# Kernel optimization log

Hardware: AMD Instinct MI355X
Metric: run time of the kernel (lower is better)

The kernel has to match this reference:

```python
import jax, jax.numpy as jnp
import numpy as np


def setup_inputs() -> dict:
    key = jax.random.key(0)
    k1, k2, k3, k4 = jax.random.split(key, 4)
    B, C, H, Wd = 32, 512, 32, 32
    sparse_dim, dict_size, feature_dim = 1024, 1024, 512
    x = jax.random.normal(k1, (B, C, H, Wd), dtype=jnp.float32)
    dictionary = jax.random.normal(k2, (dict_size, feature_dim), dtype=jnp.float32)
    # scale W, S like the LISTA init (|| . || ~ O(1)) so iterates stay bounded
    W = jax.random.normal(k3, (sparse_dim, feature_dim), dtype=jnp.float32) * 0.02
    S = jax.random.normal(k4, (sparse_dim, sparse_dim), dtype=jnp.float32) * 0.02
    thresh = jnp.float32(0.1)
    return {"x": x, "dictionary": dictionary, "W": W, "S": S, "thresh": thresh, "num_steps": 5}


def _soft_threshold(z, thresh):
    return jnp.sign(z) * jnp.maximum(jnp.abs(z) - thresh, 0.0)


def reference(x, dictionary, W, S, thresh, num_steps):
    B, C, H, Wd = x.shape
    sparse_dim = S.shape[0]
    # [B,C,H,W] -> [B*H*W, C]
    x_flat = jnp.transpose(x, (0, 2, 3, 1)).reshape(-1, C)
    dict_norm = dictionary / jnp.linalg.norm(dictionary, axis=1, keepdims=True)
    # W @ x^T is loop-invariant; compute once. [K, N]
    Wx = W @ x_flat.T
    z = jnp.zeros((sparse_dim, x_flat.shape[0]), dtype=x.dtype)
    for _ in range(num_steps):
        z = z + Wx
        z = z - S @ z
        z = _soft_threshold(z, thresh)
    # [K,N] -> [B,K,H,W]
    z = jnp.transpose(z.T.reshape(B, H, Wd, sparse_dim), (0, 3, 1, 2))
    return (z, dict_norm)
```

## Files before the change

### kernel.cpp

```cpp
#include <hip/hip_runtime.h>
#include <hip/hip_bf16.h>

typedef __bf16 bf16_t;
typedef __bf16 bf16x4 __attribute__((ext_vector_type(4)));
typedef __bf16 bf16x8 __attribute__((ext_vector_type(8)));
typedef float f32x4 __attribute__((ext_vector_type(4)));

#define GLOAD_LDS16(g, l)                                                      \
  __builtin_amdgcn_global_load_lds(                                            \
      (const __attribute__((address_space(1))) void*)(g),                      \
      (__attribute__((address_space(3))) void*)(l), 16, 0, 0)

#define MFMA(a, b, c) __builtin_amdgcn_mfma_f32_16x16x32_bf16((a), (b), (c), 0, 0, 0)

__global__ __launch_bounds__(512, 2) void gemm_kernel(
    const bf16_t* __restrict__ A, const bf16_t* __restrict__ Bt,
    int Kd, int mode,
    const bf16_t* __restrict__ WxIn, bf16_t* __restrict__ UnextOrWx,
    float* __restrict__ Out, const float* __restrict__ thresh_p)
{
  __shared__ __align__(16) char smem[147456];
  bf16_t* lds = (bf16_t*)smem;

  const int tid = threadIdx.x;
  const int wid = tid >> 6, lane = tid & 63;
  const int wr = wid >> 1, wc = wid & 1;
  const int lr = lane & 15, kg = lane >> 4;

  const int per = gridDim.x >> 3;
  const int logical = (blockIdx.x & 7) * per + (blockIdx.x >> 3);
  const int tileN = (logical & 7) << 7;
  const int tileM = (logical >> 3) << 8;
  const int NT = Kd >> 6;

  size_t offA[4]; int dstA[4];
  #pragma unroll
  for (int j = 0; j < 4; ++j) {
    const int f = j * 512 + tid;
    const int row = f >> 3, u = f & 7;
    const int ug = u ^ (row & 7);
    offA[j] = (size_t)(tileM + row) * Kd + ug * 8;
    dstA[j] = f * 8;
  }
  size_t offB[2]; int dstB[2];
  #pragma unroll
  for (int j = 0; j < 2; ++j) {
    const int f = j * 512 + tid;
    const int col = f >> 3, u = f & 7;
    const int ug = u ^ (col & 7);
    offB[j] = (size_t)(tileN + col) * Kd + ug * 8;
    dstB[j] = 16384 + f * 8;
  }

  auto readA = [&](int mi, int ks, int bs) -> bf16x8 {
    const int R = wr * 64 + mi * 16 + lr;
    const int ul = (ks * 4 + kg) ^ (R & 7);
    return *(const bf16x8*)(lds + bs + R * 64 + ul * 8);
  };
  auto readB = [&](int ni, int ks, int bs) -> bf16x8 {
    const int C = wc * 64 + ni * 16 + lr;
    const int ul = (ks * 4 + kg) ^ (C & 7);
    return *(const bf16x8*)(lds + bs + 16384 + C * 64 + ul * 8);
  };

  f32x4 acc[4][4] = {};
  bf16x8 af[4], bfr[4];

  #pragma unroll
  for (int j = 0; j < 4; ++j) GLOAD_LDS16(A + offA[j], lds + dstA[j]);
  #pragma unroll
  for (int j = 0; j < 2; ++j) GLOAD_LDS16(Bt + offB[j], lds + dstB[j]);
  if (NT > 1) {
    #pragma unroll
    for (int j = 0; j < 4; ++j) GLOAD_LDS16(A + offA[j] + 64, lds + 24576 + dstA[j]);
    #pragma unroll
    for (int j = 0; j < 2; ++j) GLOAD_LDS16(Bt + offB[j] + 64, lds + 24576 + dstB[j]);
  }
  asm volatile("s_waitcnt vmcnt(6)" ::: "memory");
  __builtin_amdgcn_s_barrier();

  int buf = 0, sb3 = 2;
  for (int t = 0; t < NT; ++t) {
    const int bs = buf * 24576;
    const int sbs = sb3 * 24576;
    const int ts = (t + 2 < NT) ? t + 2 : t + 2 - NT;
    const size_t ko = (size_t)ts << 6;

    #pragma unroll
    for (int mi = 0; mi < 4; ++mi) af[mi] = readA(mi, 0, bs);
    #pragma unroll
    for (int ni = 0; ni < 4; ++ni) bfr[ni] = readB(ni, 0, bs);
    GLOAD_LDS16(A + offA[0] + ko, lds + sbs + dstA[0]);
    GLOAD_LDS16(A + offA[1] + ko, lds + sbs + dstA[1]);
    GLOAD_LDS16(A + offA[2] + ko, lds + sbs + dstA[2]);
    __builtin_amdgcn_s_barrier();
    asm volatile("s_waitcnt lgkmcnt(0)" ::: "memory");
    __builtin_amdgcn_sched_barrier(0);
    __builtin_amdgcn_s_setprio(1);
    #pragma unroll
    for (int mi = 0; mi < 4; ++mi)
      #pragma unroll
      for (int ni = 0; ni < 4; ++ni)
        acc[mi][ni] = MFMA(af[mi], bfr[ni], acc[mi][ni]);
    __builtin_amdgcn_s_setprio(0);

    #pragma unroll
    for (int mi = 0; mi < 4; ++mi) af[mi] = readA(mi, 1, bs);
    #pragma unroll
    for (int ni = 0; ni < 4; ++ni) bfr[ni] = readB(ni, 1, bs);
    GLOAD_LDS16(A + offA[3] + ko, lds + sbs + dstA[3]);
    GLOAD_LDS16(Bt + offB[0] + ko, lds + sbs + dstB[0]);
    GLOAD_LDS16(Bt + offB[1] + ko, lds + sbs + dstB[1]);
    __builtin_amdgcn_s_barrier();
    asm volatile("s_waitcnt lgkmcnt(0)" ::: "memory");
    __builtin_amdgcn_sched_barrier(0);
    __builtin_amdgcn_s_setprio(1);
    #pragma unroll
    for (int mi = 0; mi < 4; ++mi)
      #pragma unroll
      for (int ni = 0; ni < 4; ++ni)
        acc[mi][ni] = MFMA(af[mi], bfr[ni], acc[mi][ni]);
    __builtin_amdgcn_s_setprio(0);
    asm volatile("s_waitcnt vmcnt(6)" ::: "memory");
    __builtin_amdgcn_s_barrier();

    buf = (buf == 2) ? 0 : buf + 1;
    sb3 = (sb3 == 2) ? 0 : sb3 + 1;
  }

  const float th = *thresh_p;

  if (mode <= 1) {
    asm volatile("s_waitcnt vmcnt(0)" ::: "memory");
    __syncthreads();
    float* Tl = (float*)smem;
    #pragma unroll
    for (int c = 0; c < 8; ++c) {
      if (c) __syncthreads();
      if (wr == (c >> 1)) {
        #pragma unroll
        for (int mj = 0; mj < 2; ++mj) {
          const int mi = (c & 1) * 2 + mj;
          const int rl = mj * 16 + kg * 4;
          #pragma unroll
          for (int ni = 0; ni < 4; ++ni) {
            const int cl = wc * 64 + ni * 16 + lr;
            #pragma unroll
            for (int r = 0; r < 4; ++r)
              Tl[(rl + r) * 132 + cl] = acc[mi][ni][r];
          }
        }
      }
      __syncthreads();
      #pragma unroll
      for (int j = 0; j < 2; ++j) {
        const int f  = j * 512 + tid;
        const int rl = f >> 5;
        const int c4 = (f & 31) * 4;
        const f32x4 v = *(const f32x4*)&Tl[rl * 132 + c4];
        const int grow = tileM + c * 32 + rl;
        const size_t gidx = (size_t)grow * 1024 + tileN + c4;
        bf16x4 ov;
        if (mode == 1) {
          const bf16x4 wx = *(const bf16x4*)&WxIn[gidx];
          #pragma unroll
          for (int e = 0; e < 4; ++e) {
            const float a  = fabsf(v[e]) - th;
            const float zn = (a > 0.f) ? copysignf(a, v[e]) : 0.f;
            ov[e] = (bf16_t)(zn + (float)wx[e]);
          }
        } else {
          #pragma unroll
          for (int e = 0; e < 4; ++e) ov[e] = (bf16_t)v[e];
        }
        *(bf16x4*)&UnextOrWx[gidx] = ov;
      }
    }
  } else {
    #pragma unroll
    for (int mi = 0; mi < 4; ++mi)
      #pragma unroll
      for (int ni = 0; ni < 4; ++ni)
        #pragma unroll
        for (int r = 0; r < 4; ++r) {
          const float v = acc[mi][ni][r];
          const float a = fabsf(v) - th;
          acc[mi][ni][r] = (a > 0.f) ? copysignf(a, v) : 0.f;
        }
    asm volatile("s_waitcnt vmcnt(0)" ::: "memory");
    __syncthreads();
    float* T = (float*)smem;
    const int    bb    = tileM >> 10;
    const size_t obase = (size_t)bb * 1048576 + (size_t)(tileM & 1023);
    #pragma unroll
    for (int ch = 0; ch < 4; ++ch) {
      if (ch) __syncthreads();
      if (wc == (ch >> 1)) {
        #pragma unroll
        for (int nj = 0; nj < 2; ++nj) {
          const int ni = (ch & 1) * 2 + nj;
          const int cp = nj * 16 + lr;
          #pragma unroll
          for (int mi = 0; mi < 4; ++mi)
            #pragma unroll
            for (int r = 0; r < 4; ++r)
              T[cp * 260 + wr * 64 + mi * 16 + kg * 4 + r] = acc[mi][ni][r];
        }
      }
      __syncthreads();
      #pragma unroll
      for (int j = 0; j < 4; ++j) {
        const int f  = j * 512 + tid;
        const int cp = f >> 6;
        const int p4 = (f & 63) * 4;
        const f32x4 v = *(const f32x4*)&T[cp * 260 + p4];
        *(f32x4*)&Out[obase + (size_t)(tileN + ch * 32 + cp) * 1024 + p4] = v;
      }
    }
  }
}

__global__ void cast_f32_bf16_kernel(const float* __restrict__ src,
                                     bf16_t* __restrict__ dst, int n) {
  int i = blockIdx.x * blockDim.x + threadIdx.x;
  if (i < n) dst[i] = (bf16_t)src[i];
}

__global__ void make_T_kernel(const float* __restrict__ S,
                              bf16_t* __restrict__ T) {
  const int idx = blockIdx.x * blockDim.x + threadIdx.x;
  const int i = idx >> 10, j = idx & 1023;
  T[idx] = (bf16_t)(((i == j) ? 1.0f : 0.0f) - S[idx]);
}

__global__ void transpose_cast_x_kernel(const float* __restrict__ x,
                                        bf16_t* __restrict__ xt) {
  __shared__ float t[32][33];
  const int b  = blockIdx.z;
  const int p0 = blockIdx.x * 32;
  const int c0 = blockIdx.y * 32;
  const int tx = threadIdx.x, ty = threadIdx.y;
  #pragma unroll
  for (int i = 0; i < 32; i += 8)
    t[ty + i][tx] = x[((size_t)b * 512 + c0 + ty + i) * 1024 + p0 + tx];
  __syncthreads();
  #pragma unroll
  for (int i = 0; i < 32; i += 8)
    xt[((size_t)b * 1024 + p0 + ty + i) * 512 + c0 + tx] = (bf16_t)t[tx][ty + i];
}

__global__ void dict_norm_kernel(const float* __restrict__ dict,
                                 float* __restrict__ out) {
  const int row = blockIdx.x;
  const int tid = threadIdx.x;
  const float* r = dict + (size_t)row * 512;
  float s = 0.f;
  for (int i = tid; i < 512; i += 256) { float v = r[i]; s += v * v; }
  #pragma unroll
  for (int off = 32; off > 0; off >>= 1) s += __shfl_down(s, off);
  __shared__ float ps[4];
  if ((tid & 63) == 0) ps[tid >> 6] = s;
  __syncthreads();
  const float inv = 1.0f / sqrtf(ps[0] + ps[1] + ps[2] + ps[3]);
  for (int i = tid; i < 512; i += 256) out[(size_t)row * 512 + i] = r[i] * inv;
}

extern "C" void kernel_launch(void* const* d_in, const int* in_sizes, int n_in,
                              void* d_out, int out_size, void* d_ws, size_t ws_size,
                              hipStream_t stream) {
  const float* x      = (const float*)d_in[0];
  const float* dict   = (const float*)d_in[1];
  const float* W      = (const float*)d_in[2];
  const float* S      = (const float*)d_in[3];
  const float* thresh = (const float*)d_in[4];

  float* out = (float*)d_out;

  char* ws = (char*)d_ws;
  bf16_t* uA   = (bf16_t*)ws;
  bf16_t* uB   = (bf16_t*)(ws + 67108864);
  bf16_t* WxBf = (bf16_t*)(ws + 134217728);
  bf16_t* xt   = (bf16_t*)(ws + 201326592);
  bf16_t* Wbf  = (bf16_t*)(ws + 234881024);
  bf16_t* Tbf  = (bf16_t*)(ws + 235929600);

  float* dnorm = out + 33554432;

  cast_f32_bf16_kernel<<<dim3(2048), dim3(256), 0, stream>>>(W, Wbf, 524288);
  make_T_kernel<<<dim3(2048), dim3(512), 0, stream>>>(S, Tbf);
  transpose_cast_x_kernel<<<dim3(32, 16, 32), dim3(32, 8), 0, stream>>>(x, xt);
  dict_norm_kernel<<<dim3(1024), dim3(256), 0, stream>>>(dict, dnorm);

  gemm_kernel<<<dim3(1024), dim3(512), 0, stream>>>(
      xt, Wbf, 512, 0, nullptr, WxBf, nullptr, thresh);

  bf16_t* uc = WxBf; bf16_t* un = uA;
  for (int s = 0; s < 4; ++s) {
    gemm_kernel<<<dim3(1024), dim3(512), 0, stream>>>(
        uc, Tbf, 1024, 1, WxBf, un, nullptr, thresh);
    uc = un;
    un = (uc == uA) ? uB : uA;
  }
  gemm_kernel<<<dim3(1024), dim3(512), 0, stream>>>(
      uc, Tbf, 1024, 2, nullptr, nullptr, out, thresh);
}
```

Before: 550.1 us.

## Fold first LISTA step into x·(TW)ᵀ GEMM and widen tiles to 256x256

Precomputes TW = (I-S)·W with a small GEMM so the first iteration becomes a K=512 GEMM over x instead of a K=1024 GEMM over Wx, saving work on one of the large GEMMs. The GEMM tile also grows from 256x128 to 256x256 with double buffering in place of triple buffering, which raises per-block data reuse and halves the grid. The wider epilogue now uses 8-wide bf16 stores. In exchange it uses the output buffer as scratch, may lower occupancy, and the pipeline waits on vmcnt(0) every step, exposing more load latency.

```diff
diff --git a/kernel.cpp b/kernel.cpp
--- a/kernel.cpp
+++ b/kernel.cpp
@@ -2,7 +2,6 @@
 #include <hip/hip_bf16.h>
 
 typedef __bf16 bf16_t;
-typedef __bf16 bf16x4 __attribute__((ext_vector_type(4)));
 typedef __bf16 bf16x8 __attribute__((ext_vector_type(8)));
 typedef float f32x4 __attribute__((ext_vector_type(4)));
 
@@ -15,11 +14,11 @@
 
 __global__ __launch_bounds__(512, 2) void gemm_kernel(
     const bf16_t* __restrict__ A, const bf16_t* __restrict__ Bt,
-    int Kd, int mode,
+    int Kd, int Nc, int mode,
     const bf16_t* __restrict__ WxIn, bf16_t* __restrict__ UnextOrWx,
     float* __restrict__ Out, const float* __restrict__ thresh_p)
 {
-  __shared__ __align__(16) char smem[147456];
+  __shared__ __align__(16) char smem[131072];
   bf16_t* lds = (bf16_t*)smem;
 
   const int tid = threadIdx.x;
@@ -29,26 +28,20 @@
 
   const int per = gridDim.x >> 3;
   const int logical = (blockIdx.x & 7) * per + (blockIdx.x >> 3);
-  const int tileN = (logical & 7) << 7;
-  const int tileM = (logical >> 3) << 8;
+  const int ntn = Nc >> 8;
+  const int tileN = (logical % ntn) << 8;
+  const int tileM = (logical / ntn) << 8;
   const int NT = Kd >> 6;
 
-  size_t offA[4]; int dstA[4];
+  int offA[4], offB[4], dstA[4], dstB[4];
   #pragma unroll
   for (int j = 0; j < 4; ++j) {
     const int f = j * 512 + tid;
     const int row = f >> 3, u = f & 7;
     const int ug = u ^ (row & 7);
-    offA[j] = (size_t)(tileM + row) * Kd + ug * 8;
+    offA[j] = (tileM + row) * Kd + ug * 8;
+    offB[j] = (tileN + row) * Kd + ug * 8;
     dstA[j] = f * 8;
-  }
-  size_t offB[2]; int dstB[2];
-  #pragma unroll
-  for (int j = 0; j < 2; ++j) {
-    const int f = j * 512 + tid;
-    const int col = f >> 3, u = f & 7;
-    const int ug = u ^ (col & 7);
-    offB[j] = (size_t)(tileN + col) * Kd + ug * 8;
     dstB[j] = 16384 + f * 8;
   }
 
@@ -58,74 +51,63 @@
     return *(const bf16x8*)(lds + bs + R * 64 + ul * 8);
   };
   auto readB = [&](int ni, int ks, int bs) -> bf16x8 {
-    const int C = wc * 64 + ni * 16 + lr;
+    const int C = wc * 128 + ni * 16 + lr;
     const int ul = (ks * 4 + kg) ^ (C & 7);
     return *(const bf16x8*)(lds + bs + 16384 + C * 64 + ul * 8);
   };
 
-  f32x4 acc[4][4] = {};
-  bf16x8 af[4], bfr[4];
+  f32x4 acc[4][8] = {};
+  bf16x8 af[4], bfr[8];
 
   #pragma unroll
   for (int j = 0; j < 4; ++j) GLOAD_LDS16(A + offA[j], lds + dstA[j]);
   #pragma unroll
-  for (int j = 0; j < 2; ++j) GLOAD_LDS16(Bt + offB[j], lds + dstB[j]);
-  if (NT > 1) {
-    #pragma unroll
-    for (int j = 0; j < 4; ++j) GLOAD_LDS16(A + offA[j] + 64, lds + 24576 + dstA[j]);
-    #pragma unroll
-    for (int j = 0; j < 2; ++j) GLOAD_LDS16(Bt + offB[j] + 64, lds + 24576 + dstB[j]);
-  }
-  asm volatile("s_waitcnt vmcnt(6)" ::: "memory");
+  for (int j = 0; j < 4; ++j) GLOAD_LDS16(Bt + offB[j], lds + dstB[j]);
+  asm volatile("s_waitcnt vmcnt(0)" ::: "memory");
   __builtin_amdgcn_s_barrier();
 
-  int buf = 0, sb3 = 2;
   for (int t = 0; t < NT; ++t) {
-    const int bs = buf * 24576;
-    const int sbs = sb3 * 24576;
-    const int ts = (t + 2 < NT) ? t + 2 : t + 2 - NT;
-    const size_t ko = (size_t)ts << 6;
-
-    #pragma unroll
-    for (int mi = 0; mi < 4; ++mi) af[mi] = readA(mi, 0, bs);
-    #pragma unroll
-    for (int ni = 0; ni < 4; ++ni) bfr[ni] = readB(ni, 0, bs);
+    const int bs  = (t & 1) << 15;
+    const int sbs = bs ^ 32768;
+    const int ts = (t + 1 < NT) ? t + 1 : 0;
+    const int ko = ts << 6;
+
     GLOAD_LDS16(A + offA[0] + ko, lds + sbs + dstA[0]);
     GLOAD_LDS16(A + offA[1] + ko, lds + sbs + dstA[1]);
     GLOAD_LDS16(A + offA[2] + ko, lds + sbs + dstA[2]);
-    __builtin_amdgcn_s_barrier();
-    asm volatile("s_waitcnt lgkmcnt(0)" ::: "memory");
-    __builtin_amdgcn_sched_barrier(0);
+    GLOAD_LDS16(A + offA[3] + ko, lds + sbs + dstA[3]);
+
+    #pragma unroll
+    for (int mi = 0; mi < 4; ++mi) af[mi] = readA(mi, 0, bs);
+    #pragma unroll
+    for (int ni = 0; ni < 8; ++ni) bfr[ni] = readB(ni, 0, bs);
     __builtin_amdgcn_s_setprio(1);
     #pragma unroll
     for (int mi = 0; mi < 4; ++mi)
       #pragma unroll
-      for (int ni = 0; ni < 4; ++ni)
+      for (int ni = 0; ni < 8; ++ni)
         acc[mi][ni] = MFMA(af[mi], bfr[ni], acc[mi][ni]);
     __builtin_amdgcn_s_setprio(0);
 
-    #pragma unroll
-    for (int mi = 0; mi < 4; ++mi) af[mi] = readA(mi, 1, bs);
-    #pragma unroll
-    for (int ni = 0; ni < 4; ++ni) bfr[ni] = readB(ni, 1, bs);
-    GLOAD_LDS16(A + offA[3] + ko, lds + sbs + dstA[3]);
     GLOAD_LDS16(Bt + offB[0] + ko, lds + sbs + dstB[0]);
     GLOAD_LDS16(Bt + offB[1] + ko, lds + sbs + dstB[1]);
-    __builtin_amdgcn_s_barrier();
-    asm volatile("s_waitcnt lgkmcnt(0)" ::: "memory");
-    __builtin_amdgcn_sched_barrier(0);
+    GLOAD_LDS16(Bt + offB[2] + ko, lds + sbs + dstB[2]);
+    GLOAD_LDS16(Bt + offB[3] + ko, lds + sbs + dstB[3]);
+
+    #pragma unroll
+    for (int mi = 0; mi < 4; ++mi) af[mi] = readA(mi, 1, bs);
+    #pragma unroll
+    for (int ni = 0; ni < 8; ++ni) bfr[ni] = readB(ni, 1, bs);
     __builtin_amdgcn_s_setprio(1);
     #pragma unroll
     for (int mi = 0; mi < 4; ++mi)
       #pragma unroll
-      for (int ni = 0; ni < 4; ++ni)
+      for (int ni = 0; ni < 8; ++ni)
         acc[mi][ni] = MFMA(af[mi], bfr[ni], acc[mi][ni]);
     __builtin_amdgcn_s_setprio(0);
-    asm volatile("s_waitcnt vmcnt(6)" ::: "memory");
+
+    asm volatile("s_waitcnt vmcnt(0)" ::: "memory");
     __builtin_amdgcn_s_barrier();
-
-    buf = (buf == 2) ? 0 : buf + 1;
-    sb3 = (sb3 == 2) ? 0 : sb3 + 1;
   }
 
   const float th = *thresh_p;
@@ -143,11 +125,11 @@
           const int mi = (c & 1) * 2 + mj;
           const int rl = mj * 16 + kg * 4;
           #pragma unroll
-          for (int ni = 0; ni < 4; ++ni) {
-            const int cl = wc * 64 + ni * 16 + lr;
+          for (int ni = 0; ni < 8; ++ni) {
+            const int cl = wc * 128 + ni * 16 + lr;
             #pragma unroll
             for (int r = 0; r < 4; ++r)
-              Tl[(rl + r) * 132 + cl] = acc[mi][ni][r];
+              Tl[(rl + r) * 260 + cl] = acc[mi][ni][r];
           }
         }
       }
@@ -156,31 +138,33 @@
       for (int j = 0; j < 2; ++j) {
         const int f  = j * 512 + tid;
         const int rl = f >> 5;
-        const int c4 = (f & 31) * 4;
-        const f32x4 v = *(const f32x4*)&Tl[rl * 132 + c4];
+        const int c8 = (f & 31) * 8;
+        float v[8];
+        *(f32x4*)&v[0] = *(const f32x4*)&Tl[rl * 260 + c8];
+        *(f32x4*)&v[4] = *(const f32x4*)&Tl[rl * 260 + c8 + 4];
         const int grow = tileM + c * 32 + rl;
-        const size_t gidx = (size_t)grow * 1024 + tileN + c4;
-        bf16x4 ov;
+        const size_t gidx = (size_t)grow * Nc + tileN + c8;
+        bf16x8 ov;
         if (mode == 1) {
-          const bf16x4 wx = *(const bf16x4*)&WxIn[gidx];
+          const bf16x8 wx = *(const bf16x8*)&WxIn[gidx];
           #pragma unroll
-          for (int e = 0; e < 4; ++e) {
+          for (int e = 0; e < 8; ++e) {
             const float a  = fabsf(v[e]) - th;
             const float zn = (a > 0.f) ? copysignf(a, v[e]) : 0.f;
             ov[e] = (bf16_t)(zn + (float)wx[e]);
           }
         } else {
           #pragma unroll
-          for (int e = 0; e < 4; ++e) ov[e] = (bf16_t)v[e];
+          for (int e = 0; e < 8; ++e) ov[e] = (bf16_t)v[e];
         }
-        *(bf16x4*)&UnextOrWx[gidx] = ov;
+        *(bf16x8*)&UnextOrWx[gidx] = ov;
       }
     }
   } else {
     #pragma unroll
     for (int mi = 0; mi < 4; ++mi)
       #pragma unroll
-      for (int ni = 0; ni < 4; ++ni)
+      for (int ni = 0; ni < 8; ++ni)
         #pragma unroll
         for (int r = 0; r < 4; ++r) {
           const float v = acc[mi][ni][r];
@@ -189,22 +173,22 @@
         }
     asm volatile("s_waitcnt vmcnt(0)" ::: "memory");
     __syncthreads();
-    float* T = (float*)smem;
+    float* Tl = (float*)smem;
     const int    bb    = tileM >> 10;
     const size_t obase = (size_t)bb * 1048576 + (size_t)(tileM & 1023);
     #pragma unroll
-    for (int ch = 0; ch < 4; ++ch) {
+    for (int ch = 0; ch < 8; ++ch) {
       if (ch) __syncthreads();
-      if (wc == (ch >> 1)) {
+      if (wc == (ch >> 2)) {
         #pragma unroll
         for (int nj = 0; nj < 2; ++nj) {
-          const int ni = (ch & 1) * 2 + nj;
+          const int ni = (ch & 3) * 2 + nj;
           const int cp = nj * 16 + lr;
           #pragma unroll
           for (int mi = 0; mi < 4; ++mi)
             #pragma unroll
             for (int r = 0; r < 4; ++r)
-              T[cp * 260 + wr * 64 + mi * 16 + kg * 4 + r] = acc[mi][ni][r];
+              Tl[cp * 260 + wr * 64 + mi * 16 + kg * 4 + r] = acc[mi][ni][r];
         }
       }
       __syncthreads();
@@ -213,7 +197,7 @@
         const int f  = j * 512 + tid;
         const int cp = f >> 6;
         const int p4 = (f & 63) * 4;
-        const f32x4 v = *(const f32x4*)&T[cp * 260 + p4];
+        const f32x4 v = *(const f32x4*)&Tl[cp * 260 + p4];
         *(f32x4*)&Out[obase + (size_t)(tileN + ch * 32 + cp) * 1024 + p4] = v;
       }
     }
@@ -247,6 +231,21 @@
   #pragma unroll
   for (int i = 0; i < 32; i += 8)
     xt[((size_t)b * 1024 + p0 + ty + i) * 512 + c0 + tx] = (bf16_t)t[tx][ty + i];
+}
+
+__global__ void transpose_cast_w_kernel(const float* __restrict__ W,
+                                        bf16_t* __restrict__ Wt) {
+  __shared__ float t[32][33];
+  const int j0 = blockIdx.x * 32;
+  const int c0 = blockIdx.y * 32;
+  const int tx = threadIdx.x, ty = threadIdx.y;
+  #pragma unroll
+  for (int i = 0; i < 32; i += 8)
+    t[ty + i][tx] = W[(size_t)(j0 + ty + i) * 512 + c0 + tx];
+  __syncthreads();
+  #pragma unroll
+  for (int i = 0; i < 32; i += 8)
+    Wt[(size_t)(c0 + ty + i) * 1024 + j0 + tx] = (bf16_t)t[tx][ty + i];
 }
 
 __global__ void dict_norm_kernel(const float* __restrict__ dict,
@@ -284,23 +283,31 @@
   bf16_t* Wbf  = (bf16_t*)(ws + 234881024);
   bf16_t* Tbf  = (bf16_t*)(ws + 235929600);
 
+  bf16_t* WtBf = (bf16_t*)out;
+  bf16_t* TWbf = WtBf + 524288;
   float* dnorm = out + 33554432;
 
   cast_f32_bf16_kernel<<<dim3(2048), dim3(256), 0, stream>>>(W, Wbf, 524288);
   make_T_kernel<<<dim3(2048), dim3(512), 0, stream>>>(S, Tbf);
   transpose_cast_x_kernel<<<dim3(32, 16, 32), dim3(32, 8), 0, stream>>>(x, xt);
+  transpose_cast_w_kernel<<<dim3(32, 16), dim3(32, 8), 0, stream>>>(W, WtBf);
   dict_norm_kernel<<<dim3(1024), dim3(256), 0, stream>>>(dict, dnorm);
 
-  gemm_kernel<<<dim3(1024), dim3(512), 0, stream>>>(
-      xt, Wbf, 512, 0, nullptr, WxBf, nullptr, thresh);
-
-  bf16_t* uc = WxBf; bf16_t* un = uA;
-  for (int s = 0; s < 4; ++s) {
-    gemm_kernel<<<dim3(1024), dim3(512), 0, stream>>>(
-        uc, Tbf, 1024, 1, WxBf, un, nullptr, thresh);
-    uc = un;
-    un = (uc == uA) ? uB : uA;
+  gemm_kernel<<<dim3(8), dim3(512), 0, stream>>>(
+      Tbf, WtBf, 1024, 512, 0, nullptr, TWbf, nullptr, thresh);
+
+  gemm_kernel<<<dim3(512), dim3(512), 0, stream>>>(
+      xt, Wbf, 512, 1024, 0, nullptr, WxBf, nullptr, thresh);
+
+  gemm_kernel<<<dim3(512), dim3(512), 0, stream>>>(
+      xt, TWbf, 512, 1024, 1, WxBf, uA, nullptr, thresh);
+
+  bf16_t* uc = uA; bf16_t* un = uB;
+  for (int s = 0; s < 3; ++s) {
+    gemm_kernel<<<dim3(512), dim3(512), 0, stream>>>(
+        uc, Tbf, 1024, 1024, 1, WxBf, un, nullptr, thresh);
+    bf16_t* tmp = uc; uc = un; un = tmp;
   }
-  gemm_kernel<<<dim3(1024), dim3(512), 0, stream>>>(
-      uc, Tbf, 1024, 2, nullptr, nullptr, out, thresh);
-}
+  gemm_kernel<<<dim3(512), dim3(512), 0, stream>>>(
+      uc, Tbf, 1024, 1024, 2, nullptr, nullptr, out, thresh);
+}
```

Result: no change. 541.4 us (-1.6%).
